# Performance work log

Hardware: AMD Instinct MI355X
Metric: run time of the kernel (lower is better)

## Reference

```python
import jax, jax.numpy as jnp
import numpy as np

N_NODES = 100000
N_EDGES = 3200000
D_IN = 256
D_OUT = 256


def setup_inputs() -> dict:
    key = jax.random.key(0)
    k1, k2, k3, k4, k5, k6 = jax.random.split(key, 6)
    X = jax.random.normal(k1, (N_NODES, D_IN), dtype=jnp.float32)
    edge_src = jax.random.randint(k2, (N_EDGES,), 0, N_NODES, dtype=jnp.int32)
    edge_dst = jax.random.randint(k3, (N_EDGES,), 0, N_NODES, dtype=jnp.int32)
    # nonnegative edge weights, as in a normalized adjacency
    edge_val = jax.random.uniform(k4, (N_EDGES,), dtype=jnp.float32)
    stdv = 1.0 / np.sqrt(D_OUT)
    W = jax.random.uniform(k5, (D_IN, D_OUT), minval=-stdv, maxval=stdv, dtype=jnp.float32)
    b = jax.random.uniform(k6, (D_OUT,), minval=-stdv, maxval=stdv, dtype=jnp.float32)
    return {"X": X, "edge_src": edge_src, "edge_dst": edge_dst, "edge_val": edge_val, "W": W, "b": b}


def reference(X, edge_src, edge_dst, edge_val, W, b):
    # support = X @ W  (dense GEMM, [N, D_OUT])
    support = X @ W
    # output = A @ support with A in COO form: gather rows at edge_src,
    # scale by edge weight, scatter-add into edge_dst rows.
    msgs = support[edge_src] * edge_val[:, None]          # [E, D_OUT]
    out = jax.ops.segment_sum(msgs, edge_dst, num_segments=N_NODES)
    return out + b
```

## Files before the change

kernel.cpp:

```cpp
#include <hip/hip_runtime.h>


typedef __bf16 bf16;
typedef bf16 bf16x4 __attribute__((ext_vector_type(4)));
typedef bf16 bf16x8 __attribute__((ext_vector_type(8)));
typedef float f32x4 __attribute__((ext_vector_type(4)));
typedef int i32x2 __attribute__((ext_vector_type(2)));

#define D_DIM 256

__global__ void pack_w(const float* __restrict__ W, bf16* __restrict__ Wf) {
    int lane = threadIdx.x;
    int blk  = blockIdx.x;
    int kt = blk >> 4, nt = blk & 15;
    int t = lane & 15, q = lane >> 4;
    int krow = kt * 32 + q * 8;
    int col  = nt * 16 + t;
    bf16x8 v;
#pragma unroll
    for (int j = 0; j < 8; ++j)
        v[j] = (bf16)W[(size_t)(krow + j) * D_DIM + col];
    ((bf16x8*)Wf)[(size_t)blk * 64 + lane] = v;
}

__global__ void gemm_xw(const float* __restrict__ X, const bf16* __restrict__ Wf,
                        bf16* __restrict__ S, int N) {
    int wid  = blockIdx.x * 4 + (threadIdx.x >> 6);
    int base = wid * 16;
    if (base >= N) return;
    int lane = threadIdx.x & 63;
    int t = lane & 15, q = lane >> 4;

    const float* xrow = X + (size_t)(base + t) * D_DIM + q * 8;
    const bf16x8* wf = (const bf16x8*)Wf;

    f32x4 acc[16];
#pragma unroll
    for (int i = 0; i < 16; ++i) acc[i] = (f32x4){0.f, 0.f, 0.f, 0.f};

#pragma unroll
    for (int kt = 0; kt < 8; ++kt) {
        f32x4 x0 = *(const f32x4*)(xrow + kt * 32);
        f32x4 x1 = *(const f32x4*)(xrow + kt * 32 + 4);
        bf16x8 a;
        a[0] = (bf16)x0[0]; a[1] = (bf16)x0[1]; a[2] = (bf16)x0[2]; a[3] = (bf16)x0[3];
        a[4] = (bf16)x1[0]; a[5] = (bf16)x1[1]; a[6] = (bf16)x1[2]; a[7] = (bf16)x1[3];
#pragma unroll
        for (int nt = 0; nt < 16; ++nt) {
            bf16x8 bfr = wf[(size_t)(kt * 16 + nt) * 64 + lane];
            acc[nt] = __builtin_amdgcn_mfma_f32_16x16x32_bf16(a, bfr, acc[nt], 0, 0, 0);
        }
    }

#pragma unroll
    for (int nt = 0; nt < 16; ++nt) {
#pragma unroll
        for (int r = 0; r < 4; ++r) {
            S[(size_t)(base + q * 4 + r) * D_DIM + nt * 16 + t] = (bf16)acc[nt][r];
        }
    }
}

__global__ void rank_edges(const int* __restrict__ edst, int* __restrict__ counts,
                           int* __restrict__ erank, int E) {
    int gid  = blockIdx.x * blockDim.x + threadIdx.x;
    int base = gid * 8;
    if (base + 8 <= E) {
        int4 d0 = *(const int4*)(edst + base);
        int4 d1 = *(const int4*)(edst + base + 4);
        int4 r0, r1;
        r0.x = atomicAdd(&counts[d0.x], 1);
        r0.y = atomicAdd(&counts[d0.y], 1);
        r0.z = atomicAdd(&counts[d0.z], 1);
        r0.w = atomicAdd(&counts[d0.w], 1);
        r1.x = atomicAdd(&counts[d1.x], 1);
        r1.y = atomicAdd(&counts[d1.y], 1);
        r1.z = atomicAdd(&counts[d1.z], 1);
        r1.w = atomicAdd(&counts[d1.w], 1);
        *(int4*)(erank + base)     = r0;
        *(int4*)(erank + base + 4) = r1;
    } else {
        for (int e = base; e < E; ++e)
            erank[e] = atomicAdd(&counts[edst[e]], 1);
    }
}

__global__ void scan_block(const int* __restrict__ counts, int n,
                           int* __restrict__ local_ex, int* __restrict__ bsums) {
    __shared__ int lds[1024];
    int tid = threadIdx.x;
    int g = blockIdx.x * 1024 + tid;
    int v = (g < n) ? counts[g] : 0;
    lds[tid] = v;
    __syncthreads();
    for (int d = 1; d < 1024; d <<= 1) {
        int add = (tid >= d) ? lds[tid - d] : 0;
        __syncthreads();
        lds[tid] += add;
        __syncthreads();
    }
    if (g < n) local_ex[g] = lds[tid] - v;
    if (tid == 1023) bsums[blockIdx.x] = lds[tid];
}

__global__ void scan_sums(const int* __restrict__ bsums, int nb, int* __restrict__ bex) {
    __shared__ int lds[128];
    int tid = threadIdx.x;
    int v = (tid < nb) ? bsums[tid] : 0;
    lds[tid] = v;
    __syncthreads();
    for (int d = 1; d < 128; d <<= 1) {
        int add = (tid >= d) ? lds[tid - d] : 0;
        __syncthreads();
        lds[tid] += add;
        __syncthreads();
    }
    if (tid < nb) bex[tid] = lds[tid] - v;
}

__global__ void add_base(int* __restrict__ off, const int* __restrict__ bex,
                         int n, int E) {
    int g = blockIdx.x * 1024 + threadIdx.x;
    if (g < n) off[g] += bex[blockIdx.x];
    if (g == 0) off[n] = E;
}

__global__ void scatter_edges(const int* __restrict__ esrc, const int* __restrict__ edst,
                              const float* __restrict__ evals, const int* __restrict__ erank,
                              const int* __restrict__ off, i32x2* __restrict__ eP, int E) {
    int gid  = blockIdx.x * blockDim.x + threadIdx.x;
    int base = gid * 8;
    if (base + 8 <= E) {
        int4 s0 = *(const int4*)(esrc + base);
        int4 s1 = *(const int4*)(esrc + base + 4);
        int4 d0 = *(const int4*)(edst + base);
        int4 d1 = *(const int4*)(edst + base + 4);
        int4 r0 = *(const int4*)(erank + base);
        int4 r1 = *(const int4*)(erank + base + 4);
        float4 v0 = *(const float4*)(evals + base);
        float4 v1 = *(const float4*)(evals + base + 4);
        int p0 = off[d0.x] + r0.x;
        int p1 = off[d0.y] + r0.y;
        int p2 = off[d0.z] + r0.z;
        int p3 = off[d0.w] + r0.w;
        int p4 = off[d1.x] + r1.x;
        int p5 = off[d1.y] + r1.y;
        int p6 = off[d1.z] + r1.z;
        int p7 = off[d1.w] + r1.w;
        eP[p0] = (i32x2){s0.x, __float_as_int(v0.x)};
        eP[p1] = (i32x2){s0.y, __float_as_int(v0.y)};
        eP[p2] = (i32x2){s0.z, __float_as_int(v0.z)};
        eP[p3] = (i32x2){s0.w, __float_as_int(v0.w)};
        eP[p4] = (i32x2){s1.x, __float_as_int(v1.x)};
        eP[p5] = (i32x2){s1.y, __float_as_int(v1.y)};
        eP[p6] = (i32x2){s1.z, __float_as_int(v1.z)};
        eP[p7] = (i32x2){s1.w, __float_as_int(v1.w)};
    } else {
        for (int e = base; e < E; ++e) {
            eP[off[edst[e]] + erank[e]] = (i32x2){esrc[e], __float_as_int(evals[e])};
        }
    }
}

__global__ void __launch_bounds__(256) aggregate(
        const bf16* __restrict__ S, const int* __restrict__ off,
        const i32x2* __restrict__ eP, const float* __restrict__ b,
        float* __restrict__ out, int N) {
    int w = blockIdx.x * 4 + (threadIdx.x >> 6);
    if (w >= N) return;
    int lane = threadIdx.x & 63;

    f32x4 acc = ((const f32x4*)b)[lane];

    int e   = off[w];
    int end = off[w + 1];

    for (; e + 16 <= end; e += 16) {
        i32x2 r[16];
#pragma unroll
        for (int j = 0; j < 16; ++j) r[j] = __builtin_nontemporal_load(&eP[e + j]);
        bf16x4 v[16];
#pragma unroll
        for (int j = 0; j < 16; ++j)
            v[j] = *((const bf16x4*)(S + (size_t)r[j][0] * D_DIM) + lane);
#pragma unroll
        for (int j = 0; j < 16; ++j) {
            float wt = __int_as_float(r[j][1]);
            acc[0] += wt * (float)v[j][0];
            acc[1] += wt * (float)v[j][1];
            acc[2] += wt * (float)v[j][2];
            acc[3] += wt * (float)v[j][3];
        }
    }
    for (; e + 4 <= end; e += 4) {
        i32x2 r[4];
#pragma unroll
        for (int j = 0; j < 4; ++j) r[j] = __builtin_nontemporal_load(&eP[e + j]);
        bf16x4 v[4];
#pragma unroll
        for (int j = 0; j < 4; ++j)
            v[j] = *((const bf16x4*)(S + (size_t)r[j][0] * D_DIM) + lane);
#pragma unroll
        for (int j = 0; j < 4; ++j) {
            float wt = __int_as_float(r[j][1]);
            acc[0] += wt * (float)v[j][0];
            acc[1] += wt * (float)v[j][1];
            acc[2] += wt * (float)v[j][2];
            acc[3] += wt * (float)v[j][3];
        }
    }
    for (; e < end; ++e) {
        i32x2 r = eP[e];
        float wt = __int_as_float(r[1]);
        bf16x4 v = *((const bf16x4*)(S + (size_t)r[0] * D_DIM) + lane);
        acc[0] += wt * (float)v[0];
        acc[1] += wt * (float)v[1];
        acc[2] += wt * (float)v[2];
        acc[3] += wt * (float)v[3];
    }
    __builtin_nontemporal_store(acc, (f32x4*)out + (size_t)w * 64 + lane);
}

extern "C" void kernel_launch(void* const* d_in, const int* in_sizes, int n_in,
                              void* d_out, int out_size, void* d_ws, size_t ws_size,
                              hipStream_t stream) {
    const float* X     = (const float*)d_in[0];
    const int*   esrc  = (const int*)d_in[1];
    const int*   edst  = (const int*)d_in[2];
    const float* evals = (const float*)d_in[3];
    const float* W     = (const float*)d_in[4];
    const float* bias  = (const float*)d_in[5];
    float* out = (float*)d_out;

    const int N = in_sizes[0] / D_DIM;
    const int E = in_sizes[1];

    auto alignup = [](size_t x) { return (x + 255) & ~(size_t)255; };
    char* ws = (char*)d_ws;
    size_t o = 0;
    bf16* S      = (bf16*)(ws + o); o = alignup(o + (size_t)N * D_DIM * sizeof(bf16));
    int* counts  = (int*)(ws + o);  o = alignup(o + (size_t)N * sizeof(int));
    int* off     = (int*)(ws + o);  o = alignup(o + (size_t)(N + 1) * sizeof(int));
    int* erank   = (int*)(ws + o);  o = alignup(o + (size_t)E * sizeof(int));
    int* bsums   = (int*)(ws + o);  o = alignup(o + 1024 * sizeof(int));
    int* bex     = (int*)(ws + o);  o = alignup(o + 1024 * sizeof(int));
    i32x2* eP    = (i32x2*)(ws + o); o = alignup(o + (size_t)E * sizeof(i32x2));
    bf16* Wf     = (bf16*)(ws + o); o = alignup(o + (size_t)D_DIM * D_DIM * sizeof(bf16));

    const int nb = (N + 1023) / 1024;
    const int nwaves = (N + 15) / 16;
    const int nthr8 = (E + 7) / 8;

    hipMemsetAsync(counts, 0, (size_t)N * sizeof(int), stream);
    pack_w<<<128, 64, 0, stream>>>(W, Wf);
    gemm_xw<<<(nwaves + 3) / 4, 256, 0, stream>>>(X, Wf, S, N);
    rank_edges<<<(nthr8 + 255) / 256, 256, 0, stream>>>(edst, counts, erank, E);
    scan_block<<<nb, 1024, 0, stream>>>(counts, N, off, bsums);
    scan_sums<<<1, 128, 0, stream>>>(bsums, nb, bex);
    add_base<<<nb, 1024, 0, stream>>>(off, bex, N, E);
    scatter_edges<<<(nthr8 + 255) / 256, 256, 0, stream>>>(esrc, edst, evals, erank, off, eP, E);
    aggregate<<<(N + 3) / 4, 256, 0, stream>>>(S, off, eP, bias, out, N);
}
```

Baseline: 664.2 us.

## Bucket edges by source range and destination group for register-resident aggregation

Edges are now sorted by a two-level key: one of 32 source-node buckets, then one of 2048 destination groups of 49 nodes. The source node index and the local destination offset are packed into one word. Each wave keeps 49 per-node accumulators in registers, selects the right one with a wave-uniform switch, and walks the source buckets in order. The aim is to make the row gathers from S more cache-local across waves. The cost is very high register pressure, a branchy switch on every edge, and only 2048 waves in flight, which may leave too little parallelism to hide the latency of the gathers.

```diff
diff --git a/kernel.cpp b/kernel.cpp
--- a/kernel.cpp
+++ b/kernel.cpp
@@ -8,6 +8,17 @@
 typedef int i32x2 __attribute__((ext_vector_type(2)));
 
 #define D_DIM 256
+#define NB 32
+#define NGRP 2048
+#define G 49
+
+__device__ __forceinline__ int bucket_of(unsigned s, unsigned magic) {
+    unsigned b = (unsigned)(((unsigned long long)s * magic) >> 32);
+    return b > (NB - 1) ? (NB - 1) : (int)b;
+}
+__device__ __forceinline__ int wgroup_of(unsigned d, unsigned m49) {
+    return (int)(((unsigned long long)d * m49) >> 32);
+}
 
 __global__ void pack_w(const float* __restrict__ W, bf16* __restrict__ Wf) {
     int lane = threadIdx.x;
@@ -61,27 +72,31 @@
     }
 }
 
-__global__ void rank_edges(const int* __restrict__ edst, int* __restrict__ counts,
-                           int* __restrict__ erank, int E) {
+__global__ void rank4(const int* __restrict__ esrc, const int* __restrict__ edst,
+                      int* __restrict__ cnt, int* __restrict__ erank, int E,
+                      unsigned bmagic, unsigned m49) {
     int gid  = blockIdx.x * blockDim.x + threadIdx.x;
     int base = gid * 8;
     if (base + 8 <= E) {
+        int4 s0 = *(const int4*)(esrc + base);
+        int4 s1 = *(const int4*)(esrc + base + 4);
         int4 d0 = *(const int4*)(edst + base);
         int4 d1 = *(const int4*)(edst + base + 4);
         int4 r0, r1;
-        r0.x = atomicAdd(&counts[d0.x], 1);
-        r0.y = atomicAdd(&counts[d0.y], 1);
-        r0.z = atomicAdd(&counts[d0.z], 1);
-        r0.w = atomicAdd(&counts[d0.w], 1);
-        r1.x = atomicAdd(&counts[d1.x], 1);
-        r1.y = atomicAdd(&counts[d1.y], 1);
-        r1.z = atomicAdd(&counts[d1.z], 1);
-        r1.w = atomicAdd(&counts[d1.w], 1);
+        r0.x = atomicAdd(&cnt[bucket_of(s0.x, bmagic) * NGRP + wgroup_of(d0.x, m49)], 1);
+        r0.y = atomicAdd(&cnt[bucket_of(s0.y, bmagic) * NGRP + wgroup_of(d0.y, m49)], 1);
+        r0.z = atomicAdd(&cnt[bucket_of(s0.z, bmagic) * NGRP + wgroup_of(d0.z, m49)], 1);
+        r0.w = atomicAdd(&cnt[bucket_of(s0.w, bmagic) * NGRP + wgroup_of(d0.w, m49)], 1);
+        r1.x = atomicAdd(&cnt[bucket_of(s1.x, bmagic) * NGRP + wgroup_of(d1.x, m49)], 1);
+        r1.y = atomicAdd(&cnt[bucket_of(s1.y, bmagic) * NGRP + wgroup_of(d1.y, m49)], 1);
+        r1.z = atomicAdd(&cnt[bucket_of(s1.z, bmagic) * NGRP + wgroup_of(d1.z, m49)], 1);
+        r1.w = atomicAdd(&cnt[bucket_of(s1.w, bmagic) * NGRP + wgroup_of(d1.w, m49)], 1);
         *(int4*)(erank + base)     = r0;
         *(int4*)(erank + base + 4) = r1;
     } else {
         for (int e = base; e < E; ++e)
-            erank[e] = atomicAdd(&counts[edst[e]], 1);
+            erank[e] = atomicAdd(
+                &cnt[bucket_of(esrc[e], bmagic) * NGRP + wgroup_of(edst[e], m49)], 1);
     }
 }
 
@@ -125,9 +140,10 @@
     if (g == 0) off[n] = E;
 }
 
-__global__ void scatter_edges(const int* __restrict__ esrc, const int* __restrict__ edst,
-                              const float* __restrict__ evals, const int* __restrict__ erank,
-                              const int* __restrict__ off, i32x2* __restrict__ eP, int E) {
+__global__ void scatter4(const int* __restrict__ esrc, const int* __restrict__ edst,
+                         const float* __restrict__ evals, const int* __restrict__ erank,
+                         const int* __restrict__ off, i32x2* __restrict__ eP, int E,
+                         unsigned bmagic, unsigned m49) {
     int gid  = blockIdx.x * blockDim.x + threadIdx.x;
     int base = gid * 8;
     if (base + 8 <= E) {
@@ -139,86 +155,83 @@
         int4 r1 = *(const int4*)(erank + base + 4);
         float4 v0 = *(const float4*)(evals + base);
         float4 v1 = *(const float4*)(evals + base + 4);
-        int p0 = off[d0.x] + r0.x;
-        int p1 = off[d0.y] + r0.y;
-        int p2 = off[d0.z] + r0.z;
-        int p3 = off[d0.w] + r0.w;
-        int p4 = off[d1.x] + r1.x;
-        int p5 = off[d1.y] + r1.y;
-        int p6 = off[d1.z] + r1.z;
-        int p7 = off[d1.w] + r1.w;
-        eP[p0] = (i32x2){s0.x, __float_as_int(v0.x)};
-        eP[p1] = (i32x2){s0.y, __float_as_int(v0.y)};
-        eP[p2] = (i32x2){s0.z, __float_as_int(v0.z)};
-        eP[p3] = (i32x2){s0.w, __float_as_int(v0.w)};
-        eP[p4] = (i32x2){s1.x, __float_as_int(v1.x)};
-        eP[p5] = (i32x2){s1.y, __float_as_int(v1.y)};
-        eP[p6] = (i32x2){s1.z, __float_as_int(v1.z)};
-        eP[p7] = (i32x2){s1.w, __float_as_int(v1.w)};
+        int ss[8] = {s0.x, s0.y, s0.z, s0.w, s1.x, s1.y, s1.z, s1.w};
+        int dd[8] = {d0.x, d0.y, d0.z, d0.w, d1.x, d1.y, d1.z, d1.w};
+        int rr[8] = {r0.x, r0.y, r0.z, r0.w, r1.x, r1.y, r1.z, r1.w};
+        float vv[8] = {v0.x, v0.y, v0.z, v0.w, v1.x, v1.y, v1.z, v1.w};
+#pragma unroll
+        for (int j = 0; j < 8; ++j) {
+            int wg = wgroup_of(dd[j], m49);
+            int dl = dd[j] - wg * G;
+            int key = bucket_of(ss[j], bmagic) * NGRP + wg;
+            int pos = off[key] + rr[j];
+            eP[pos] = (i32x2){ss[j] | (dl << 20), __float_as_int(vv[j])};
+        }
     } else {
         for (int e = base; e < E; ++e) {
-            eP[off[edst[e]] + erank[e]] = (i32x2){esrc[e], __float_as_int(evals[e])};
-        }
-    }
-}
-
-__global__ void __launch_bounds__(256) aggregate(
-        const bf16* __restrict__ S, const int* __restrict__ off,
+            int wg = wgroup_of(edst[e], m49);
+            int dl = edst[e] - wg * G;
+            int key = bucket_of(esrc[e], bmagic) * NGRP + wg;
+            int pos = off[key] + erank[e];
+            eP[pos] = (i32x2){esrc[e] | (dl << 20), __float_as_int(evals[e])};
+        }
+    }
+}
+
+#define APPLY(P, V) {                                                        \
+    unsigned px = (unsigned)(P)[0];                                          \
+    float wt = __int_as_float((P)[1]);                                       \
+    float f0 = wt * (float)(V)[0], f1 = wt * (float)(V)[1],                  \
+          f2 = wt * (float)(V)[2], f3 = wt * (float)(V)[3];                  \
+    switch (px >> 20) {                                                      \
+        CASE(0) CASE(1) CASE(2) CASE(3) CASE(4) CASE(5) CASE(6) CASE(7)      \
+        CASE(8) CASE(9) CASE(10) CASE(11) CASE(12) CASE(13) CASE(14)         \
+        CASE(15) CASE(16) CASE(17) CASE(18) CASE(19) CASE(20) CASE(21)       \
+        CASE(22) CASE(23) CASE(24) CASE(25) CASE(26) CASE(27) CASE(28)       \
+        CASE(29) CASE(30) CASE(31) CASE(32) CASE(33) CASE(34) CASE(35)       \
+        CASE(36) CASE(37) CASE(38) CASE(39) CASE(40) CASE(41) CASE(42)       \
+        CASE(43) CASE(44) CASE(45) CASE(46) CASE(47) CASE(48)                \
+    } }
+#define CASE(i) case i: acc[i][0]+=f0; acc[i][1]+=f1; acc[i][2]+=f2; acc[i][3]+=f3; break;
+
+__global__ void __launch_bounds__(256, 2) aggregate4(
+        const bf16* __restrict__ S, const int* __restrict__ off4,
         const i32x2* __restrict__ eP, const float* __restrict__ b,
         float* __restrict__ out, int N) {
-    int w = blockIdx.x * 4 + (threadIdx.x >> 6);
-    if (w >= N) return;
+    int wid  = threadIdx.x >> 6;
     int lane = threadIdx.x & 63;
-
-    f32x4 acc = ((const f32x4*)b)[lane];
-
-    int e   = off[w];
-    int end = off[w + 1];
-
-    for (; e + 16 <= end; e += 16) {
-        i32x2 r[16];
-#pragma unroll
-        for (int j = 0; j < 16; ++j) r[j] = __builtin_nontemporal_load(&eP[e + j]);
-        bf16x4 v[16];
-#pragma unroll
-        for (int j = 0; j < 16; ++j)
-            v[j] = *((const bf16x4*)(S + (size_t)r[j][0] * D_DIM) + lane);
-#pragma unroll
-        for (int j = 0; j < 16; ++j) {
-            float wt = __int_as_float(r[j][1]);
-            acc[0] += wt * (float)v[j][0];
-            acc[1] += wt * (float)v[j][1];
-            acc[2] += wt * (float)v[j][2];
-            acc[3] += wt * (float)v[j][3];
-        }
-    }
-    for (; e + 4 <= end; e += 4) {
-        i32x2 r[4];
-#pragma unroll
-        for (int j = 0; j < 4; ++j) r[j] = __builtin_nontemporal_load(&eP[e + j]);
-        bf16x4 v[4];
-#pragma unroll
-        for (int j = 0; j < 4; ++j)
-            v[j] = *((const bf16x4*)(S + (size_t)r[j][0] * D_DIM) + lane);
-#pragma unroll
-        for (int j = 0; j < 4; ++j) {
-            float wt = __int_as_float(r[j][1]);
-            acc[0] += wt * (float)v[j][0];
-            acc[1] += wt * (float)v[j][1];
-            acc[2] += wt * (float)v[j][2];
-            acc[3] += wt * (float)v[j][3];
-        }
-    }
-    for (; e < end; ++e) {
-        i32x2 r = eP[e];
-        float wt = __int_as_float(r[1]);
-        bf16x4 v = *((const bf16x4*)(S + (size_t)r[0] * D_DIM) + lane);
-        acc[0] += wt * (float)v[0];
-        acc[1] += wt * (float)v[1];
-        acc[2] += wt * (float)v[2];
-        acc[3] += wt * (float)v[3];
-    }
-    __builtin_nontemporal_store(acc, (f32x4*)out + (size_t)w * 64 + lane);
+    int w    = blockIdx.x * 4 + wid;
+
+    const f32x4 bias = ((const f32x4*)b)[lane];
+    f32x4 acc[G];
+#pragma unroll
+    for (int i = 0; i < G; ++i) acc[i] = bias;
+
+    for (int k = 0; k < NB; ++k) {
+        int s = off4[k * NGRP + w];
+        int t = off4[k * NGRP + w + 1];
+        int e = s;
+        for (; e + 4 <= t; e += 4) {
+            i32x2 p0 = eP[e], p1 = eP[e + 1], p2 = eP[e + 2], p3 = eP[e + 3];
+            bf16x4 v0 = *((const bf16x4*)(S + (size_t)(p0[0] & 0xFFFFF) * D_DIM) + lane);
+            bf16x4 v1 = *((const bf16x4*)(S + (size_t)(p1[0] & 0xFFFFF) * D_DIM) + lane);
+            bf16x4 v2 = *((const bf16x4*)(S + (size_t)(p2[0] & 0xFFFFF) * D_DIM) + lane);
+            bf16x4 v3 = *((const bf16x4*)(S + (size_t)(p3[0] & 0xFFFFF) * D_DIM) + lane);
+            APPLY(p0, v0) APPLY(p1, v1) APPLY(p2, v2) APPLY(p3, v3)
+        }
+        for (; e < t; ++e) {
+            i32x2 p = eP[e];
+            bf16x4 v = *((const bf16x4*)(S + (size_t)(p[0] & 0xFFFFF) * D_DIM) + lane);
+            APPLY(p, v)
+        }
+    }
+
+#pragma unroll
+    for (int i = 0; i < G; ++i) {
+        int node = w * G + i;
+        if (node < N)
+            __builtin_nontemporal_store(acc[i], (f32x4*)out + (size_t)node * 64 + lane);
+    }
 }
 
 extern "C" void kernel_launch(void* const* d_in, const int* in_sizes, int n_in,
@@ -235,29 +248,33 @@
     const int N = in_sizes[0] / D_DIM;
     const int E = in_sizes[1];
 
+    const int M2 = NB * NGRP;
+    const unsigned bmagic = (unsigned)((((unsigned long long)NB << 32) + N - 1) / N);
+    const unsigned m49 = (unsigned)((((unsigned long long)1 << 32) + G - 1) / G);
+
     auto alignup = [](size_t x) { return (x + 255) & ~(size_t)255; };
     char* ws = (char*)d_ws;
     size_t o = 0;
     bf16* S      = (bf16*)(ws + o); o = alignup(o + (size_t)N * D_DIM * sizeof(bf16));
-    int* counts  = (int*)(ws + o);  o = alignup(o + (size_t)N * sizeof(int));
-    int* off     = (int*)(ws + o);  o = alignup(o + (size_t)(N + 1) * sizeof(int));
+    int* cnt4    = (int*)(ws + o);  o = alignup(o + (size_t)(M2 + 16) * sizeof(int));
+    int* off4    = (int*)(ws + o);  o = alignup(o + (size_t)(M2 + 16) * sizeof(int));
     int* erank   = (int*)(ws + o);  o = alignup(o + (size_t)E * sizeof(int));
     int* bsums   = (int*)(ws + o);  o = alignup(o + 1024 * sizeof(int));
     int* bex     = (int*)(ws + o);  o = alignup(o + 1024 * sizeof(int));
     i32x2* eP    = (i32x2*)(ws + o); o = alignup(o + (size_t)E * sizeof(i32x2));
     bf16* Wf     = (bf16*)(ws + o); o = alignup(o + (size_t)D_DIM * D_DIM * sizeof(bf16));
 
-    const int nb = (N + 1023) / 1024;
     const int nwaves = (N + 15) / 16;
-    const int nthr8 = (E + 7) / 8;
-
-    hipMemsetAsync(counts, 0, (size_t)N * sizeof(int), stream);
+    const int nb8    = ((E + 7) / 8 + 255) / 256;
+    const int nbs    = (M2 + 1023) / 1024;
+
+    hipMemsetAsync(cnt4, 0, (size_t)(M2 + 16) * sizeof(int), stream);
     pack_w<<<128, 64, 0, stream>>>(W, Wf);
     gemm_xw<<<(nwaves + 3) / 4, 256, 0, stream>>>(X, Wf, S, N);
-    rank_edges<<<(nthr8 + 255) / 256, 256, 0, stream>>>(edst, counts, erank, E);
-    scan_block<<<nb, 1024, 0, stream>>>(counts, N, off, bsums);
-    scan_sums<<<1, 128, 0, stream>>>(bsums, nb, bex);
-    add_base<<<nb, 1024, 0, stream>>>(off, bex, N, E);
-    scatter_edges<<<(nthr8 + 255) / 256, 256, 0, stream>>>(esrc, edst, evals, erank, off, eP, E);
-    aggregate<<<(N + 3) / 4, 256, 0, stream>>>(S, off, eP, bias, out, N);
-}
+    rank4<<<nb8, 256, 0, stream>>>(esrc, edst, cnt4, erank, E, bmagic, m49);
+    scan_block<<<nbs, 1024, 0, stream>>>(cnt4, M2, off4, bsums);
+    scan_sums<<<1, 128, 0, stream>>>(bsums, nbs, bex);
+    add_base<<<nbs, 1024, 0, stream>>>(off4, bex, M2, E);
+    scatter4<<<nb8, 256, 0, stream>>>(esrc, edst, evals, erank, off4, eP, E, bmagic, m49);
+    aggregate4<<<NGRP / 4, 256, 0, stream>>>(S, off4, eP, bias, out, N);
+}
```

Result: slower. 997.4 us (+50.2%).

## Fuse GEMM with edge ranking and fold scan base-add into consumers

Applied to the files above, without the earlier changes.

Merges the X@W GEMM and the atomic edge-ranking pass into one launch that interleaves blocks by parity, so compute-bound MFMA work and atomic-heavy ranking run concurrently. It also removes the add_base kernel by having scatter_edges and aggregate add the per-1024-block scan offset on the fly. The scan now covers N+1 entries so the end offset comes out of the scan itself. This saves two launches and lets the two independent phases overlap, at the cost of an extra small gather per edge and per node.

```diff
diff --git a/kernel.cpp b/kernel.cpp
--- a/kernel.cpp
+++ b/kernel.cpp
@@ -6,6 +6,7 @@
 typedef bf16 bf16x8 __attribute__((ext_vector_type(8)));
 typedef float f32x4 __attribute__((ext_vector_type(4)));
 typedef int i32x2 __attribute__((ext_vector_type(2)));
+typedef int i32x4 __attribute__((ext_vector_type(4)));
 
 #define D_DIM 256
 
@@ -23,9 +24,34 @@
     ((bf16x8*)Wf)[(size_t)blk * 64 + lane] = v;
 }
 
-__global__ void gemm_xw(const float* __restrict__ X, const bf16* __restrict__ Wf,
-                        bf16* __restrict__ S, int N) {
-    int wid  = blockIdx.x * 4 + (threadIdx.x >> 6);
+__global__ void gemm_rank(const float* __restrict__ X, const bf16* __restrict__ Wf,
+                          bf16* __restrict__ S, int N,
+                          const int* __restrict__ edst, int* __restrict__ counts,
+                          int* __restrict__ erank, int E) {
+    if (blockIdx.x & 1) {
+        int gid  = (blockIdx.x >> 1) * blockDim.x + threadIdx.x;
+        int base = gid * 8;
+        if (base + 8 <= E) {
+            int4 d0 = *(const int4*)(edst + base);
+            int4 d1 = *(const int4*)(edst + base + 4);
+            int4 r0, r1;
+            r0.x = atomicAdd(&counts[d0.x], 1);
+            r0.y = atomicAdd(&counts[d0.y], 1);
+            r0.z = atomicAdd(&counts[d0.z], 1);
+            r0.w = atomicAdd(&counts[d0.w], 1);
+            r1.x = atomicAdd(&counts[d1.x], 1);
+            r1.y = atomicAdd(&counts[d1.y], 1);
+            r1.z = atomicAdd(&counts[d1.z], 1);
+            r1.w = atomicAdd(&counts[d1.w], 1);
+            *(int4*)(erank + base)     = r0;
+            *(int4*)(erank + base + 4) = r1;
+        } else {
+            for (int e = base; e < E; ++e)
+                erank[e] = atomicAdd(&counts[edst[e]], 1);
+        }
+        return;
+    }
+    int wid  = (blockIdx.x >> 1) * 4 + (threadIdx.x >> 6);
     int base = wid * 16;
     if (base >= N) return;
     int lane = threadIdx.x & 63;
@@ -58,30 +84,6 @@
         for (int r = 0; r < 4; ++r) {
             S[(size_t)(base + q * 4 + r) * D_DIM + nt * 16 + t] = (bf16)acc[nt][r];
         }
-    }
-}
-
-__global__ void rank_edges(const int* __restrict__ edst, int* __restrict__ counts,
-                           int* __restrict__ erank, int E) {
-    int gid  = blockIdx.x * blockDim.x + threadIdx.x;
-    int base = gid * 8;
-    if (base + 8 <= E) {
-        int4 d0 = *(const int4*)(edst + base);
-        int4 d1 = *(const int4*)(edst + base + 4);
-        int4 r0, r1;
-        r0.x = atomicAdd(&counts[d0.x], 1);
-        r0.y = atomicAdd(&counts[d0.y], 1);
-        r0.z = atomicAdd(&counts[d0.z], 1);
-        r0.w = atomicAdd(&counts[d0.w], 1);
-        r1.x = atomicAdd(&counts[d1.x], 1);
-        r1.y = atomicAdd(&counts[d1.y], 1);
-        r1.z = atomicAdd(&counts[d1.z], 1);
-        r1.w = atomicAdd(&counts[d1.w], 1);
-        *(int4*)(erank + base)     = r0;
-        *(int4*)(erank + base + 4) = r1;
-    } else {
-        for (int e = base; e < E; ++e)
-            erank[e] = atomicAdd(&counts[edst[e]], 1);
     }
 }
 
@@ -118,16 +120,10 @@
     if (tid < nb) bex[tid] = lds[tid] - v;
 }
 
-__global__ void add_base(int* __restrict__ off, const int* __restrict__ bex,
-                         int n, int E) {
-    int g = blockIdx.x * 1024 + threadIdx.x;
-    if (g < n) off[g] += bex[blockIdx.x];
-    if (g == 0) off[n] = E;
-}
-
 __global__ void scatter_edges(const int* __restrict__ esrc, const int* __restrict__ edst,
                               const float* __restrict__ evals, const int* __restrict__ erank,
-                              const int* __restrict__ off, i32x2* __restrict__ eP, int E) {
+                              const int* __restrict__ off, const int* __restrict__ bex,
+                              i32x2* __restrict__ eP, int E) {
     int gid  = blockIdx.x * blockDim.x + threadIdx.x;
     int base = gid * 8;
     if (base + 8 <= E) {
@@ -139,14 +135,14 @@
         int4 r1 = *(const int4*)(erank + base + 4);
         float4 v0 = *(const float4*)(evals + base);
         float4 v1 = *(const float4*)(evals + base + 4);
-        int p0 = off[d0.x] + r0.x;
-        int p1 = off[d0.y] + r0.y;
-        int p2 = off[d0.z] + r0.z;
-        int p3 = off[d0.w] + r0.w;
-        int p4 = off[d1.x] + r1.x;
-        int p5 = off[d1.y] + r1.y;
-        int p6 = off[d1.z] + r1.z;
-        int p7 = off[d1.w] + r1.w;
+        int p0 = off[d0.x] + bex[d0.x >> 10] + r0.x;
+        int p1 = off[d0.y] + bex[d0.y >> 10] + r0.y;
+        int p2 = off[d0.z] + bex[d0.z >> 10] + r0.z;
+        int p3 = off[d0.w] + bex[d0.w >> 10] + r0.w;
+        int p4 = off[d1.x] + bex[d1.x >> 10] + r1.x;
+        int p5 = off[d1.y] + bex[d1.y >> 10] + r1.y;
+        int p6 = off[d1.z] + bex[d1.z >> 10] + r1.z;
+        int p7 = off[d1.w] + bex[d1.w >> 10] + r1.w;
         eP[p0] = (i32x2){s0.x, __float_as_int(v0.x)};
         eP[p1] = (i32x2){s0.y, __float_as_int(v0.y)};
         eP[p2] = (i32x2){s0.z, __float_as_int(v0.z)};
@@ -157,23 +153,25 @@
         eP[p7] = (i32x2){s1.w, __float_as_int(v1.w)};
     } else {
         for (int e = base; e < E; ++e) {
-            eP[off[edst[e]] + erank[e]] = (i32x2){esrc[e], __float_as_int(evals[e])};
+            int d = edst[e];
+            eP[off[d] + bex[d >> 10] + erank[e]] =
+                (i32x2){esrc[e], __float_as_int(evals[e])};
         }
     }
 }
 
 __global__ void __launch_bounds__(256) aggregate(
         const bf16* __restrict__ S, const int* __restrict__ off,
-        const i32x2* __restrict__ eP, const float* __restrict__ b,
-        float* __restrict__ out, int N) {
+        const int* __restrict__ bex, const i32x2* __restrict__ eP,
+        const float* __restrict__ b, float* __restrict__ out, int N) {
     int w = blockIdx.x * 4 + (threadIdx.x >> 6);
     if (w >= N) return;
     int lane = threadIdx.x & 63;
 
     f32x4 acc = ((const f32x4*)b)[lane];
 
-    int e   = off[w];
-    int end = off[w + 1];
+    int e   = off[w]     + bex[w >> 10];
+    int end = off[w + 1] + bex[(w + 1) >> 10];
 
     for (; e + 16 <= end; e += 16) {
         i32x2 r[16];
@@ -239,7 +237,7 @@
     char* ws = (char*)d_ws;
     size_t o = 0;
     bf16* S      = (bf16*)(ws + o); o = alignup(o + (size_t)N * D_DIM * sizeof(bf16));
-    int* counts  = (int*)(ws + o);  o = alignup(o + (size_t)N * sizeof(int));
+    int* counts  = (int*)(ws + o);  o = alignup(o + (size_t)(N + 1) * sizeof(int));
     int* off     = (int*)(ws + o);  o = alignup(o + (size_t)(N + 1) * sizeof(int));
     int* erank   = (int*)(ws + o);  o = alignup(o + (size_t)E * sizeof(int));
     int* bsums   = (int*)(ws + o);  o = alignup(o + 1024 * sizeof(int));
@@ -247,17 +245,17 @@
     i32x2* eP    = (i32x2*)(ws + o); o = alignup(o + (size_t)E * sizeof(i32x2));
     bf16* Wf     = (bf16*)(ws + o); o = alignup(o + (size_t)D_DIM * D_DIM * sizeof(bf16));
 
-    const int nb = (N + 1023) / 1024;
-    const int nwaves = (N + 15) / 16;
-    const int nthr8 = (E + 7) / 8;
-
-    hipMemsetAsync(counts, 0, (size_t)N * sizeof(int), stream);
+    const int nb = (N + 1 + 1023) / 1024;
+    const int nwaves  = (N + 15) / 16;
+    const int ngemmb  = (nwaves + 3) / 4;
+    const int nrankb  = ((E + 7) / 8 + 255) / 256;
+    const int nfused  = 2 * ((ngemmb > nrankb) ? ngemmb : nrankb);
+
+    hipMemsetAsync(counts, 0, (size_t)(N + 1) * sizeof(int), stream);
     pack_w<<<128, 64, 0, stream>>>(W, Wf);
-    gemm_xw<<<(nwaves + 3) / 4, 256, 0, stream>>>(X, Wf, S, N);
-    rank_edges<<<(nthr8 + 255) / 256, 256, 0, stream>>>(edst, counts, erank, E);
-    scan_block<<<nb, 1024, 0, stream>>>(counts, N, off, bsums);
+    gemm_rank<<<nfused, 256, 0, stream>>>(X, Wf, S, N, edst, counts, erank, E);
+    scan_block<<<nb, 1024, 0, stream>>>(counts, N + 1, off, bsums);
     scan_sums<<<1, 128, 0, stream>>>(bsums, nb, bex);
-    add_base<<<nb, 1024, 0, stream>>>(off, bex, N, E);
-    scatter_edges<<<(nthr8 + 255) / 256, 256, 0, stream>>>(esrc, edst, evals, erank, off, eP, E);
-    aggregate<<<(N + 3) / 4, 256, 0, stream>>>(S, off, eP, bias, out, N);
-}
+    scatter_edges<<<nrankb, 256, 0, stream>>>(esrc, edst, evals, erank, off, bex, eP, E);
+    aggregate<<<(N + 3) / 4, 256, 0, stream>>>(S, off, bex, eP, bias, out, N);
+}
```

New measurement: 631.5 us. -4.9%, faster.
